# Kernel tuning notes

Measured on AMD Instinct MI355X. Metric: run time of the kernel, lower is better.

## Reference

```python
import jax, jax.numpy as jnp
import numpy as np

N_NODES = 50000
N_EDGES = 800000
D_IN = 128
D_OUT = 128
ALPHA = 0.5


def setup_inputs() -> dict:
    key = jax.random.key(0)
    k1, k2, k3, k4, k5, k6 = jax.random.split(key, 6)
    x = jax.random.normal(k1, (N_NODES, D_IN), dtype=jnp.float32)
    edge_index = jax.random.randint(k2, (2, N_EDGES), 0, N_NODES, dtype=jnp.int32)
    s = 1.0 / np.sqrt(D_IN)  # torch.nn.Linear default init bound
    W_src = jax.random.uniform(k3, (D_IN, D_OUT), jnp.float32, -s, s)
    b_src = jax.random.uniform(k4, (D_OUT,), jnp.float32, -s, s)
    W_dst = jax.random.uniform(k5, (D_IN, D_OUT), jnp.float32, -s, s)
    b_dst = jax.random.uniform(k6, (D_OUT,), jnp.float32, -s, s)
    return {"x": x, "edge_index": edge_index, "W_src": W_src, "b_src": b_src,
            "W_dst": W_dst, "b_dst": b_dst}


def reference(x, edge_index, W_src, b_src, W_dst, b_dst):
    row, col = edge_index[0], edge_index[1]
    ones = jnp.ones((row.shape[0],), dtype=x.dtype)
    # out-degree = row sums of A; in-degree = column sums of A
    out_deg = jax.ops.segment_sum(ones, row, num_segments=N_NODES)
    in_deg = jax.ops.segment_sum(ones, col, num_segments=N_NODES)
    d_out = jnp.where(out_deg > 0, out_deg ** -0.5, 0.0)
    d_in = jnp.where(in_deg > 0, in_deg ** -0.5, 0.0)
    # D_out^{-1/2} A D_in^{-1/2}: per-edge weight. For A^T the normalized
    # weight at (col,row) is d_in[col]*d_out[row] == same weight, transposed scatter.
    w = d_out[row] * d_in[col]  # [E]
    msg_fwd = w[:, None] * x[col]  # [E, D_IN]
    agg_fwd = jax.ops.segment_sum(msg_fwd, row, num_segments=N_NODES)  # adj_norm @ x
    msg_bwd = w[:, None] * x[row]
    agg_bwd = jax.ops.segment_sum(msg_bwd, col, num_segments=N_NODES)  # adj_t_norm @ x
    out = ALPHA * (agg_fwd @ W_src + b_src) + (1.0 - ALPHA) * (agg_bwd @ W_dst + b_dst)
    return out
```

## Files before the change

### kernel.cpp

```cpp
#include <hip/hip_runtime.h>
#include <hip/hip_bf16.h>


constexpr int N_NODES = 50000;
constexpr int N_EDGES = 800000;
constexpr int D = 128;
constexpr int CAP = 48;
constexpr int NPBK = 128;
constexpr int NBUK = (N_NODES + NPBK - 1) / NPBK;
constexpr int ECH = 2048;
constexpr int NCH = (N_EDGES + ECH - 1) / ECH;
constexpr int CAPB = 2600;
constexpr int CVTB = 2048;

typedef __bf16 bf16x8 __attribute__((ext_vector_type(8)));
typedef float  f32x4  __attribute__((ext_vector_type(4)));

__global__ __launch_bounds__(256) void k_part(const int* __restrict__ row,
                                              const int* __restrict__ col,
                                              int* __restrict__ tail,
                                              unsigned* __restrict__ part,
                                              const float* __restrict__ Wsrc,
                                              const float* __restrict__ Wdst,
                                              __hip_bfloat16* __restrict__ Wpk,
                                              const float* __restrict__ x,
                                              __hip_bfloat16* __restrict__ xb) {
    const int bid = blockIdx.x;
    if (bid < CVTB) {
        const float4* x4 = (const float4*)x;
        bf16x8* xb8 = (bf16x8*)xb;
        const int stride = CVTB * 256;
        for (int i = bid * 256 + threadIdx.x; i < N_NODES * D / 8; i += stride) {
            float4 v0 = x4[2 * i];
            float4 v1 = x4[2 * i + 1];
            union { bf16x8 v; __hip_bfloat16 e[8]; } u;
            u.e[0] = __float2bfloat16(v0.x); u.e[1] = __float2bfloat16(v0.y);
            u.e[2] = __float2bfloat16(v0.z); u.e[3] = __float2bfloat16(v0.w);
            u.e[4] = __float2bfloat16(v1.x); u.e[5] = __float2bfloat16(v1.y);
            u.e[6] = __float2bfloat16(v1.z); u.e[7] = __float2bfloat16(v1.w);
            xb8[i] = u.v;
        }
        return;
    }
    if (bid >= CVTB + NCH * 2) {
        int t = (bid - CVTB - NCH * 2) * 256 + threadIdx.x;
        int f = t >> 6;
        int lane = t & 63;
        int dir = f >> 5;
        int ct = (f >> 2) & 7;
        int ks = f & 3;
        const float* W = dir ? Wdst : Wsrc;
        int k0 = ks * 32 + (lane >> 4) * 8;
        int n = ct * 16 + (lane & 15);
        __hip_bfloat16 v[8];
        #pragma unroll
        for (int j = 0; j < 8; ++j) v[j] = __float2bfloat16(W[(k0 + j) * D + n]);
        *(bf16x8*)&Wpk[(size_t)t * 8] = *(const bf16x8*)v;
        return;
    }
    __shared__ int cnt[NBUK], base[NBUK], pos[NBUK];
    const int task = bid - CVTB;
    const int dir = task & 1;
    const int chunk = task >> 1;
    const int* dst = dir ? col : row;
    const int* src = dir ? row : col;
    for (int i = threadIdx.x; i < NBUK; i += 256) { cnt[i] = 0; pos[i] = 0; }
    __syncthreads();
    const int e0 = chunk * ECH;
    const int e1 = min(e0 + ECH, N_EDGES);
    for (int e = e0 + threadIdx.x; e < e1; e += 256)
        atomicAdd(&cnt[dst[e] >> 7], 1);
    __syncthreads();
    for (int i = threadIdx.x; i < NBUK; i += 256)
        base[i] = (cnt[i] > 0) ? atomicAdd(&tail[dir * NBUK + i], cnt[i]) : 0;
    __syncthreads();
    for (int e = e0 + threadIdx.x; e < e1; e += 256) {
        int d = dst[e], s = src[e];
        int b = d >> 7;
        int p = base[b] + atomicAdd(&pos[b], 1);
        if (p < CAPB)
            part[((size_t)dir * NBUK + b) * CAPB + p] =
                ((unsigned)(d & (NPBK - 1)) << 16) | (unsigned)s;
    }
}

__global__ __launch_bounds__(256) void k_bin(const int* __restrict__ tail,
                                             const unsigned* __restrict__ part,
                                             unsigned short* __restrict__ binF,
                                             unsigned short* __restrict__ binB,
                                             int* __restrict__ cntF,
                                             int* __restrict__ cntB,
                                             float* __restrict__ sc_row,
                                             float* __restrict__ sc_col) {
    __shared__ alignas(16) unsigned short bins[NPBK * CAP];
    __shared__ int cnt[NPBK];
    const int dir = blockIdx.x & 1;
    const int b = blockIdx.x >> 1;
    for (int i = threadIdx.x; i < NPBK; i += 256) cnt[i] = 0;
    __syncthreads();
    const int n = min(tail[dir * NBUK + b], CAPB);
    const unsigned* p = &part[((size_t)dir * NBUK + b) * CAPB];
    for (int i = threadIdx.x; i < n; i += 256) {
        unsigned ent = p[i];
        int dl = ent >> 16;
        int q = atomicAdd(&cnt[dl], 1);
        if (q < CAP) bins[dl * CAP + q] = (unsigned short)(ent & 0xFFFFu);
    }
    __syncthreads();
    unsigned short* gbin = dir ? binB : binF;
    int* gcnt = dir ? cntB : cntF;
    float* sc = dir ? sc_col : sc_row;
    const int node0 = b * NPBK;
    const int nv = min(NPBK, N_NODES - node0);
    const int nq = nv * (CAP * 2 / 16);
    const uint4* bw = (const uint4*)bins;
    uint4* gw = (uint4*)&gbin[(size_t)node0 * CAP];
    for (int i = threadIdx.x; i < nq; i += 256) gw[i] = bw[i];
    for (int i = threadIdx.x; i < nv; i += 256) {
        int c = cnt[i];
        gcnt[node0 + i] = c;
        sc[node0 + i] = (c > 0) ? rsqrtf((float)c) : 0.f;
    }
}

__global__ __launch_bounds__(256) void k_aggemm(const unsigned short* __restrict__ binF,
                                                const int* __restrict__ cntF,
                                                const unsigned short* __restrict__ binB,
                                                const int* __restrict__ cntB,
                                                const float* __restrict__ sc_row,
                                                const float* __restrict__ sc_col,
                                                const uint2* __restrict__ xb2,
                                                const bf16x8* __restrict__ Wpk,
                                                const float* __restrict__ b_src,
                                                const float* __restrict__ b_dst,
                                                float* __restrict__ out) {
    __shared__ alignas(16) __hip_bfloat16 As[2][16][136];
    const int wave = threadIdx.x >> 6;
    const int lane = threadIdx.x & 63;
    const int half = lane >> 5;
    const int l32 = lane & 31;
    const int tile = blockIdx.x;

    for (int r4 = 0; r4 < 4; ++r4) {
        const int lr = wave * 4 + r4;
        const int node = tile * 16 + lr;
        const int nF = min(cntF[node], CAP);
        const int nB = min(cntB[node], CAP);

        int entF = (lane < nF) ? (int)binF[(size_t)node * CAP + lane] : 0;
        int entB = (lane < nB) ? (int)binB[(size_t)node * CAP + lane] : 0;
        float sclF = sc_col[entF];
        float sclB = sc_row[entB];

        const int sTailF = __shfl(entF, (nF > 0) ? nF - 1 : 0);
        const int sTailB = __shfl(entB, (nB > 0) ? nB - 1 : 0);
        const float wTailF = __shfl(sclF, (nF > 0) ? nF - 1 : 0);
        const float wTailB = __shfl(sclB, (nB > 0) ? nB - 1 : 0);

        float4 accF = make_float4(0.f, 0.f, 0.f, 0.f);
        {
            const int npair = nF >> 1;
            int i = 0;
            for (; i + 3 < npair; i += 4) {
                int s0 = __shfl(entF, 2 * i + half);
                int s1 = __shfl(entF, 2 * (i + 1) + half);
                int s2 = __shfl(entF, 2 * (i + 2) + half);
                int s3 = __shfl(entF, 2 * (i + 3) + half);
                float w0 = __shfl(sclF, 2 * i + half);
                float w1 = __shfl(sclF, 2 * (i + 1) + half);
                float w2 = __shfl(sclF, 2 * (i + 2) + half);
                float w3 = __shfl(sclF, 2 * (i + 3) + half);
                uint2 v0 = xb2[(size_t)s0 * 32 + l32];
                uint2 v1 = xb2[(size_t)s1 * 32 + l32];
                uint2 v2 = xb2[(size_t)s2 * 32 + l32];
                uint2 v3 = xb2[(size_t)s3 * 32 + l32];
                union { unsigned u; float f; } a, b;
                a.u = v0.x << 16; b.u = v0.x & 0xFFFF0000u;
                accF.x += w0 * a.f; accF.y += w0 * b.f;
                a.u = v0.y << 16; b.u = v0.y & 0xFFFF0000u;
                accF.z += w0 * a.f; accF.w += w0 * b.f;
                a.u = v1.x << 16; b.u = v1.x & 0xFFFF0000u;
                accF.x += w1 * a.f; accF.y += w1 * b.f;
                a.u = v1.y << 16; b.u = v1.y & 0xFFFF0000u;
                accF.z += w1 * a.f; accF.w += w1 * b.f;
                a.u = v2.x << 16; b.u = v2.x & 0xFFFF0000u;
                accF.x += w2 * a.f; accF.y += w2 * b.f;
                a.u = v2.y << 16; b.u = v2.y & 0xFFFF0000u;
                accF.z += w2 * a.f; accF.w += w2 * b.f;
                a.u = v3.x << 16; b.u = v3.x & 0xFFFF0000u;
                accF.x += w3 * a.f; accF.y += w3 * b.f;
                a.u = v3.y << 16; b.u = v3.y & 0xFFFF0000u;
                accF.z += w3 * a.f; accF.w += w3 * b.f;
            }
            for (; i < npair; ++i) {
                int s = __shfl(entF, 2 * i + half);
                float w = __shfl(sclF, 2 * i + half);
                uint2 v = xb2[(size_t)s * 32 + l32];
                union { unsigned u; float f; } a, b;
                a.u = v.x << 16; b.u = v.x & 0xFFFF0000u;
                accF.x += w * a.f; accF.y += w * b.f;
                a.u = v.y << 16; b.u = v.y & 0xFFFF0000u;
                accF.z += w * a.f; accF.w += w * b.f;
            }
            if ((nF & 1) && half == 0) {
                uint2 v = xb2[(size_t)sTailF * 32 + l32];
                union { unsigned u; float f; } a, b;
                a.u = v.x << 16; b.u = v.x & 0xFFFF0000u;
                accF.x += wTailF * a.f; accF.y += wTailF * b.f;
                a.u = v.y << 16; b.u = v.y & 0xFFFF0000u;
                accF.z += wTailF * a.f; accF.w += wTailF * b.f;
            }
        }
        float4 accB = make_float4(0.f, 0.f, 0.f, 0.f);
        {
            const int npair = nB >> 1;
            int i = 0;
            for (; i + 3 < npair; i += 4) {
                int s0 = __shfl(entB, 2 * i + half);
                int s1 = __shfl(entB, 2 * (i + 1) + half);
                int s2 = __shfl(entB, 2 * (i + 2) + half);
                int s3 = __shfl(entB, 2 * (i + 3) + half);
                float w0 = __shfl(sclB, 2 * i + half);
                float w1 = __shfl(sclB, 2 * (i + 1) + half);
                float w2 = __shfl(sclB, 2 * (i + 2) + half);
                float w3 = __shfl(sclB, 2 * (i + 3) + half);
                uint2 v0 = xb2[(size_t)s0 * 32 + l32];
                uint2 v1 = xb2[(size_t)s1 * 32 + l32];
                uint2 v2 = xb2[(size_t)s2 * 32 + l32];
                uint2 v3 = xb2[(size_t)s3 * 32 + l32];
                union { unsigned u; float f; } a, b;
                a.u = v0.x << 16; b.u = v0.x & 0xFFFF0000u;
                accB.x += w0 * a.f; accB.y += w0 * b.f;
                a.u = v0.y << 16; b.u = v0.y & 0xFFFF0000u;
                accB.z += w0 * a.f; accB.w += w0 * b.f;
                a.u = v1.x << 16; b.u = v1.x & 0xFFFF0000u;
                accB.x += w1 * a.f; accB.y += w1 * b.f;
                a.u = v1.y << 16; b.u = v1.y & 0xFFFF0000u;
                accB.z += w1 * a.f; accB.w += w1 * b.f;
                a.u = v2.x << 16; b.u = v2.x & 0xFFFF0000u;
                accB.x += w2 * a.f; accB.y += w2 * b.f;
                a.u = v2.y << 16; b.u = v2.y & 0xFFFF0000u;
                accB.z += w2 * a.f; accB.w += w2 * b.f;
                a.u = v3.x << 16; b.u = v3.x & 0xFFFF0000u;
                accB.x += w3 * a.f; accB.y += w3 * b.f;
                a.u = v3.y << 16; b.u = v3.y & 0xFFFF0000u;
                accB.z += w3 * a.f; accB.w += w3 * b.f;
            }
            for (; i < npair; ++i) {
                int s = __shfl(entB, 2 * i + half);
                float w = __shfl(sclB, 2 * i + half);
                uint2 v = xb2[(size_t)s * 32 + l32];
                union { unsigned u; float f; } a, b;
                a.u = v.x << 16; b.u = v.x & 0xFFFF0000u;
                accB.x += w * a.f; accB.y += w * b.f;
                a.u = v.y << 16; b.u = v.y & 0xFFFF0000u;
                accB.z += w * a.f; accB.w += w * b.f;
            }
            if ((nB & 1) && half == 0) {
                uint2 v = xb2[(size_t)sTailB * 32 + l32];
                union { unsigned u; float f; } a, b;
                a.u = v.x << 16; b.u = v.x & 0xFFFF0000u;
                accB.x += wTailB * a.f; accB.y += wTailB * b.f;
                a.u = v.y << 16; b.u = v.y & 0xFFFF0000u;
                accB.z += wTailB * a.f; accB.w += wTailB * b.f;
            }
        }

        accF.x += __shfl_xor(accF.x, 32);
        accF.y += __shfl_xor(accF.y, 32);
        accF.z += __shfl_xor(accF.z, 32);
        accF.w += __shfl_xor(accF.w, 32);
        accB.x += __shfl_xor(accB.x, 32);
        accB.y += __shfl_xor(accB.y, 32);
        accB.z += __shfl_xor(accB.z, 32);
        accB.w += __shfl_xor(accB.w, 32);

        if (half == 0) {
            float s = 0.5f * sc_row[node];
            union { uint2 u; __hip_bfloat16 e[4]; } rr;
            rr.e[0] = __float2bfloat16(s * accF.x);
            rr.e[1] = __float2bfloat16(s * accF.y);
            rr.e[2] = __float2bfloat16(s * accF.z);
            rr.e[3] = __float2bfloat16(s * accF.w);
            *(uint2*)&As[0][lr][l32 * 4] = rr.u;
        } else {
            float s = 0.5f * sc_col[node];
            union { uint2 u; __hip_bfloat16 e[4]; } rr;
            rr.e[0] = __float2bfloat16(s * accB.x);
            rr.e[1] = __float2bfloat16(s * accB.y);
            rr.e[2] = __float2bfloat16(s * accB.z);
            rr.e[3] = __float2bfloat16(s * accB.w);
            *(uint2*)&As[1][lr][l32 * 4] = rr.u;
        }
    }
    __syncthreads();

    const int quad = lane >> 4;
    const int m = lane & 15;
    bf16x8 aF[4], aB[4];
    #pragma unroll
    for (int ks = 0; ks < 4; ++ks) {
        aF[ks] = *(const bf16x8*)&As[0][m][ks * 32 + quad * 8];
        aB[ks] = *(const bf16x8*)&As[1][m][ks * 32 + quad * 8];
    }
    const int crow = tile * 16 + quad * 4;
    #pragma unroll
    for (int cti = 0; cti < 2; ++cti) {
        const int ct = wave * 2 + cti;
        f32x4 c = {0.f, 0.f, 0.f, 0.f};
        #pragma unroll
        for (int ks = 0; ks < 4; ++ks)
            c = __builtin_amdgcn_mfma_f32_16x16x32_bf16(aF[ks], Wpk[(ct * 4 + ks) * 64 + lane], c, 0, 0, 0);
        #pragma unroll
        for (int ks = 0; ks < 4; ++ks)
            c = __builtin_amdgcn_mfma_f32_16x16x32_bf16(aB[ks], Wpk[2048 + (ct * 4 + ks) * 64 + lane], c, 0, 0, 0);
        const int colb = ct * 16 + m;
        const float bias = 0.5f * (b_src[colb] + b_dst[colb]);
        #pragma unroll
        for (int r = 0; r < 4; ++r)
            out[(size_t)(crow + r) * D + colb] = c[r] + bias;
    }
}

extern "C" void kernel_launch(void* const* d_in, const int* in_sizes, int n_in,
                              void* d_out, int out_size, void* d_ws, size_t ws_size,
                              hipStream_t stream) {
    const float* x     = (const float*)d_in[0];
    const int*   edges = (const int*)d_in[1];
    const float* W_src = (const float*)d_in[2];
    const float* b_src = (const float*)d_in[3];
    const float* W_dst = (const float*)d_in[4];
    const float* b_dst = (const float*)d_in[5];
    float* out = (float*)d_out;

    const int* row = edges;
    const int* col = edges + N_EDGES;

    __hip_bfloat16* xb     = (__hip_bfloat16*)d_ws;
    __hip_bfloat16* Wpk    = xb + (size_t)N_NODES * D;
    float*          sc_row = (float*)(Wpk + 64 * 512);
    float*          sc_col = sc_row + N_NODES;
    int*            cntF   = (int*)(sc_col + N_NODES);
    int*            cntB   = cntF + N_NODES;
    int*            tail   = cntB + N_NODES;
    unsigned*       part   = (unsigned*)(tail + 1024);
    unsigned short* binF   = (unsigned short*)(part + (size_t)2 * NBUK * CAPB);
    unsigned short* binB   = binF + (size_t)N_NODES * CAP;

    (void)hipMemsetAsync(tail, 0, 2 * NBUK * sizeof(int), stream);

    const int gP = CVTB + NCH * 2 + 16;
    const int gB = NBUK * 2;
    const int gA = N_NODES / 16;

    k_part<<<gP, 256, 0, stream>>>(row, col, tail, part, W_src, W_dst, Wpk, x, xb);
    k_bin<<<gB, 256, 0, stream>>>(tail, part, binF, binB, cntF, cntB, sc_row, sc_col);
    k_aggemm<<<gA, 256, 0, stream>>>(binF, cntF, binB, cntB, sc_row, sc_col,
                                     (const uint2*)xb, (const bf16x8*)Wpk,
                                     b_src, b_dst, out);
}
```

Measured before the change: 186.2 us.

## Fuse per-node binning into aggregation kernel and compute degrees via global atomics

Removes the separate k_bin kernel. Degrees are now counted with global atomics in the partition kernel, and each aggregation block re-scans its 128-node bucket's partition list in shared memory to build the bins for its 16 nodes. Normalization scales are computed on the fly with rsqrt from the degree counts instead of being read from precomputed arrays. This saves a kernel launch and the global bin write/read round trip. In exchange, each bucket's partition data is read 8 times (once per sub-tile), there are 800k extra global atomics per direction, and per-neighbor degree lookups become int loads followed by rsqrt.

```diff
diff --git a/kernel.cpp b/kernel.cpp
--- a/kernel.cpp
+++ b/kernel.cpp
@@ -20,6 +20,8 @@
                                               const int* __restrict__ col,
                                               int* __restrict__ tail,
                                               unsigned* __restrict__ part,
+                                              int* __restrict__ cntF,
+                                              int* __restrict__ cntB,
                                               const float* __restrict__ Wsrc,
                                               const float* __restrict__ Wdst,
                                               __hip_bfloat16* __restrict__ Wpk,
@@ -64,12 +66,16 @@
     const int chunk = task >> 1;
     const int* dst = dir ? col : row;
     const int* src = dir ? row : col;
+    int* gdeg = dir ? cntB : cntF;
     for (int i = threadIdx.x; i < NBUK; i += 256) { cnt[i] = 0; pos[i] = 0; }
     __syncthreads();
     const int e0 = chunk * ECH;
     const int e1 = min(e0 + ECH, N_EDGES);
-    for (int e = e0 + threadIdx.x; e < e1; e += 256)
-        atomicAdd(&cnt[dst[e] >> 7], 1);
+    for (int e = e0 + threadIdx.x; e < e1; e += 256) {
+        int d = dst[e];
+        atomicAdd(&cnt[d >> 7], 1);
+        atomicAdd(&gdeg[d], 1);
+    }
     __syncthreads();
     for (int i = threadIdx.x; i < NBUK; i += 256)
         base[i] = (cnt[i] > 0) ? atomicAdd(&tail[dir * NBUK + i], cnt[i]) : 0;
@@ -84,73 +90,55 @@
     }
 }
 
-__global__ __launch_bounds__(256) void k_bin(const int* __restrict__ tail,
-                                             const unsigned* __restrict__ part,
-                                             unsigned short* __restrict__ binF,
-                                             unsigned short* __restrict__ binB,
-                                             int* __restrict__ cntF,
-                                             int* __restrict__ cntB,
-                                             float* __restrict__ sc_row,
-                                             float* __restrict__ sc_col) {
-    __shared__ alignas(16) unsigned short bins[NPBK * CAP];
-    __shared__ int cnt[NPBK];
-    const int dir = blockIdx.x & 1;
-    const int b = blockIdx.x >> 1;
-    for (int i = threadIdx.x; i < NPBK; i += 256) cnt[i] = 0;
-    __syncthreads();
-    const int n = min(tail[dir * NBUK + b], CAPB);
-    const unsigned* p = &part[((size_t)dir * NBUK + b) * CAPB];
-    for (int i = threadIdx.x; i < n; i += 256) {
-        unsigned ent = p[i];
-        int dl = ent >> 16;
-        int q = atomicAdd(&cnt[dl], 1);
-        if (q < CAP) bins[dl * CAP + q] = (unsigned short)(ent & 0xFFFFu);
-    }
-    __syncthreads();
-    unsigned short* gbin = dir ? binB : binF;
-    int* gcnt = dir ? cntB : cntF;
-    float* sc = dir ? sc_col : sc_row;
-    const int node0 = b * NPBK;
-    const int nv = min(NPBK, N_NODES - node0);
-    const int nq = nv * (CAP * 2 / 16);
-    const uint4* bw = (const uint4*)bins;
-    uint4* gw = (uint4*)&gbin[(size_t)node0 * CAP];
-    for (int i = threadIdx.x; i < nq; i += 256) gw[i] = bw[i];
-    for (int i = threadIdx.x; i < nv; i += 256) {
-        int c = cnt[i];
-        gcnt[node0 + i] = c;
-        sc[node0 + i] = (c > 0) ? rsqrtf((float)c) : 0.f;
-    }
-}
-
-__global__ __launch_bounds__(256) void k_aggemm(const unsigned short* __restrict__ binF,
+__global__ __launch_bounds__(256) void k_aggemm(const int* __restrict__ tail,
+                                                const unsigned* __restrict__ part,
                                                 const int* __restrict__ cntF,
-                                                const unsigned short* __restrict__ binB,
                                                 const int* __restrict__ cntB,
-                                                const float* __restrict__ sc_row,
-                                                const float* __restrict__ sc_col,
                                                 const uint2* __restrict__ xb2,
                                                 const bf16x8* __restrict__ Wpk,
                                                 const float* __restrict__ b_src,
                                                 const float* __restrict__ b_dst,
                                                 float* __restrict__ out) {
     __shared__ alignas(16) __hip_bfloat16 As[2][16][136];
+    __shared__ alignas(16) unsigned short lbin[2][16][CAP];
+    __shared__ int lcnt[2][16];
     const int wave = threadIdx.x >> 6;
     const int lane = threadIdx.x & 63;
     const int half = lane >> 5;
     const int l32 = lane & 31;
     const int tile = blockIdx.x;
 
+    if (threadIdx.x < 32) lcnt[threadIdx.x >> 4][threadIdx.x & 15] = 0;
+    __syncthreads();
+    const int bk = tile >> 3;
+    const int sub = tile & 7;
+    #pragma unroll
+    for (int dir = 0; dir < 2; ++dir) {
+        const int n = min(tail[dir * NBUK + bk], CAPB);
+        const unsigned* p = &part[((size_t)dir * NBUK + bk) * CAPB];
+        for (int i = threadIdx.x; i < n; i += 256) {
+            unsigned ent = p[i];
+            int dl = ent >> 16;
+            if ((dl >> 4) == sub) {
+                int q = atomicAdd(&lcnt[dir][dl & 15], 1);
+                if (q < CAP) lbin[dir][dl & 15][q] = (unsigned short)(ent & 0xFFFFu);
+            }
+        }
+    }
+    __syncthreads();
+
     for (int r4 = 0; r4 < 4; ++r4) {
         const int lr = wave * 4 + r4;
         const int node = tile * 16 + lr;
-        const int nF = min(cntF[node], CAP);
-        const int nB = min(cntB[node], CAP);
-
-        int entF = (lane < nF) ? (int)binF[(size_t)node * CAP + lane] : 0;
-        int entB = (lane < nB) ? (int)binB[(size_t)node * CAP + lane] : 0;
-        float sclF = sc_col[entF];
-        float sclB = sc_row[entB];
+        const int nF = min(lcnt[0][lr], CAP);
+        const int nB = min(lcnt[1][lr], CAP);
+
+        int entF = (lane < nF) ? (int)lbin[0][lr][lane] : 0;
+        int entB = (lane < nB) ? (int)lbin[1][lr][lane] : 0;
+        int cF = cntB[entF];
+        int cB = cntF[entB];
+        float sclF = (cF > 0) ? rsqrtf((float)cF) : 0.f;
+        float sclB = (cB > 0) ? rsqrtf((float)cB) : 0.f;
 
         const int sTailF = __shfl(entF, (nF > 0) ? nF - 1 : 0);
         const int sTailB = __shfl(entB, (nB > 0) ? nB - 1 : 0);
@@ -276,7 +264,8 @@
         accB.w += __shfl_xor(accB.w, 32);
 
         if (half == 0) {
-            float s = 0.5f * sc_row[node];
+            int dF = cntF[node];
+            float s = (dF > 0) ? 0.5f * rsqrtf((float)dF) : 0.f;
             union { uint2 u; __hip_bfloat16 e[4]; } rr;
             rr.e[0] = __float2bfloat16(s * accF.x);
             rr.e[1] = __float2bfloat16(s * accF.y);
@@ -284,7 +273,8 @@
             rr.e[3] = __float2bfloat16(s * accF.w);
             *(uint2*)&As[0][lr][l32 * 4] = rr.u;
         } else {
-            float s = 0.5f * sc_col[node];
+            int dB = cntB[node];
+            float s = (dB > 0) ? 0.5f * rsqrtf((float)dB) : 0.f;
             union { uint2 u; __hip_bfloat16 e[4]; } rr;
             rr.e[0] = __float2bfloat16(s * accB.x);
             rr.e[1] = __float2bfloat16(s * accB.y);
@@ -338,24 +328,19 @@
 
     __hip_bfloat16* xb     = (__hip_bfloat16*)d_ws;
     __hip_bfloat16* Wpk    = xb + (size_t)N_NODES * D;
-    float*          sc_row = (float*)(Wpk + 64 * 512);
-    float*          sc_col = sc_row + N_NODES;
-    int*            cntF   = (int*)(sc_col + N_NODES);
+    int*            cntF   = (int*)(Wpk + 64 * 512);
     int*            cntB   = cntF + N_NODES;
     int*            tail   = cntB + N_NODES;
-    unsigned*       part   = (unsigned*)(tail + 1024);
-    unsigned short* binF   = (unsigned short*)(part + (size_t)2 * NBUK * CAPB);
-    unsigned short* binB   = binF + (size_t)N_NODES * CAP;
-
-    (void)hipMemsetAsync(tail, 0, 2 * NBUK * sizeof(int), stream);
+    unsigned*       part   = (unsigned*)(tail + 2 * NBUK);
+
+    (void)hipMemsetAsync(cntF, 0, (2 * N_NODES + 2 * NBUK) * sizeof(int), stream);
 
     const int gP = CVTB + NCH * 2 + 16;
-    const int gB = NBUK * 2;
     const int gA = N_NODES / 16;
 
-    k_part<<<gP, 256, 0, stream>>>(row, col, tail, part, W_src, W_dst, Wpk, x, xb);
-    k_bin<<<gB, 256, 0, stream>>>(tail, part, binF, binB, cntF, cntB, sc_row, sc_col);
-    k_aggemm<<<gA, 256, 0, stream>>>(binF, cntF, binB, cntB, sc_row, sc_col,
+    k_part<<<gP, 256, 0, stream>>>(row, col, tail, part, cntF, cntB,
+                                   W_src, W_dst, Wpk, x, xb);
+    k_aggemm<<<gA, 256, 0, stream>>>(tail, part, cntF, cntB,
                                      (const uint2*)xb, (const bf16x8*)Wpk,
                                      b_src, b_dst, out);
 }
```

Result: slower. 243.0 us (+30.5%).
